# Kernel optimization log

Hardware: AMD Instinct MI355X
Metric: run time of the kernel (lower is better)

The kernel has to match this reference:

```python
import jax, jax.numpy as jnp
import numpy as np

BLOCK = 64          # block_size
R = 64              # number of OFT blocks (r)
N_ELEM = BLOCK * (BLOCK - 1) // 2  # 2016 upper-triangular elements per block
TOKENS = 8192       # batch*seq tokens
IN_FEATURES = R * BLOCK  # 4096
NUM_TERMS = 5       # num_cayley_neumann_terms

_ROWS, _COLS = jnp.triu_indices(BLOCK, k=1)


def _skew_symmetric(vec):
    # vec: [r, n_elements] -> [r, BLOCK, BLOCK] skew-symmetric
    m = jnp.zeros((vec.shape[0], BLOCK, BLOCK), dtype=vec.dtype)
    m = m.at[:, _ROWS, _COLS].set(vec)
    return m - jnp.swapaxes(m, -2, -1)


def _cayley_neumann(weight):
    # Neumann approximation of Cayley transform:
    # R = I + 2*Q + 2*Q^2 + ... + 2*Q^(NUM_TERMS-1)
    Q = _skew_symmetric(weight)                      # [r, B, B]
    eye = jnp.eye(BLOCK, dtype=weight.dtype)
    rot = eye[None, :, :] + 2.0 * Q
    Q_pow = Q
    for _ in range(2, NUM_TERMS):
        Q_pow = jnp.einsum('rij,rjk->rik', Q_pow, Q)
        rot = rot + 2.0 * Q_pow
    return rot                                        # [r, B, B]


def setup_inputs() -> dict:
    key = jax.random.key(0)
    k1, k2 = jax.random.split(key)
    x = jax.random.normal(k1, (TOKENS, IN_FEATURES), dtype=jnp.float32)
    # OFT weights start near zero (rotation ~ identity); small scale keeps
    # the Neumann series well-conditioned.
    weight = jax.random.normal(k2, (R, N_ELEM), dtype=jnp.float32) * 0.02
    return {"x": x, "weight": weight}


def reference(x, weight):
    rot = _cayley_neumann(weight)                      # [r, B, B]
    xr = x.reshape(x.shape[0], R, BLOCK)               # [n, r, B]
    out = jnp.einsum('nrk,rkc->nrc', xr, rot)          # block-diag rotation
    return out.reshape(x.shape)
```

## Files before the change

### kernel.cpp

```cpp
#include <hip/hip_runtime.h>


#define NELEM 2016

typedef __attribute__((ext_vector_type(8))) short bfrag8;
typedef __attribute__((ext_vector_type(4))) float f32x4;

__device__ __forceinline__ int triu_off(int i) {
    return i * 63 - (i * (i - 1)) / 2;
}

__device__ __forceinline__ float skew_val(const float* __restrict__ wr, int i, int j) {
    if (i < j) return  wr[triu_off(i) + (j - i - 1)];
    if (i > j) return -wr[triu_off(j) + (i - j - 1)];
    return 0.f;
}

__device__ __forceinline__ void bsplit(float v, short& h, short& l) {
    const unsigned u = __float_as_uint(v);
    h = (short)(u >> 16);
    const float resid = v - __uint_as_float(u & 0xffff0000u);
    const unsigned ur = __float_as_uint(resid);
    l = (short)((ur + 0x7fffu + ((ur >> 16) & 1u)) >> 16);
}

__global__ __launch_bounds__(256) void oft_rot_kernel(const float* __restrict__ w,
                                                      unsigned short* __restrict__ bh,
                                                      unsigned short* __restrict__ bl) {
    __shared__ float Q[64][64];
    __shared__ float Pl[2][16][65];

    const int r    = blockIdx.x;
    const int tile = blockIdx.y;
    const float* __restrict__ wr = w + r * NELEM;
    const int tid = threadIdx.x;
    const int il  = tid >> 4;
    const int j0  = (tid & 15) << 2;
    const int gi  = tile * 16 + il;

#pragma unroll
    for (int m = 0; m < 4; ++m) {
        const int i = il + 16 * m;
#pragma unroll
        for (int t = 0; t < 4; ++t)
            Q[i][j0 + t] = skew_val(wr, i, j0 + t);
    }
    __syncthreads();

    float racc[4];
#pragma unroll
    for (int t = 0; t < 4; ++t) {
        const float qv = Q[gi][j0 + t];
        Pl[0][il][j0 + t] = qv;
        racc[t] = (gi == j0 + t ? 1.f : 0.f) + 2.f * qv;
    }
    __syncthreads();

    int cur = 0;
#pragma unroll
    for (int p = 2; p < 5; ++p) {
        float a0 = 0.f, a1 = 0.f, a2 = 0.f, a3 = 0.f;
#pragma unroll 8
        for (int k = 0; k < 64; ++k) {
            const float  pv = Pl[cur][il][k];
            const float4 qv = *(const float4*)&Q[k][j0];
            a0 = fmaf(pv, qv.x, a0);
            a1 = fmaf(pv, qv.y, a1);
            a2 = fmaf(pv, qv.z, a2);
            a3 = fmaf(pv, qv.w, a3);
        }
        Pl[cur ^ 1][il][j0 + 0] = a0;
        Pl[cur ^ 1][il][j0 + 1] = a1;
        Pl[cur ^ 1][il][j0 + 2] = a2;
        Pl[cur ^ 1][il][j0 + 3] = a3;
        racc[0] += 2.f * a0;
        racc[1] += 2.f * a1;
        racc[2] += 2.f * a2;
        racc[3] += 2.f * a3;
        __syncthreads();
        cur ^= 1;
    }

    const int s    = gi >> 5;
    const int jj   = gi & 7;
    const int lhi  = ((gi >> 3) & 3) << 4;
#pragma unroll
    for (int t = 0; t < 4; ++t) {
        const int j    = j0 + t;
        const int ct   = j >> 4;
        const int lane = lhi + (j & 15);
        const int off  = (((r * 4 + ct) * 2 + s) * 64 + lane) * 8 + jj;
        short h, l;
        bsplit(racc[t], h, l);
        bh[off] = (unsigned short)h;
        bl[off] = (unsigned short)l;
    }
}

__global__ __launch_bounds__(256) void oft_apply_kernel(const float* __restrict__ x,
                                                        const unsigned short* __restrict__ bh,
                                                        const unsigned short* __restrict__ bl,
                                                        float* __restrict__ out) {
    const int tid  = threadIdx.x;
    const int w    = tid >> 6;
    const int l    = tid & 63;
    const int lrow = l & 15;
    const int lk   = l >> 4;
    const int r     = blockIdx.x;
    const int chunk = blockIdx.y;

    bfrag8 Bh[4][2], Bl[4][2];
#pragma unroll
    for (int ct = 0; ct < 4; ++ct)
#pragma unroll
        for (int s = 0; s < 2; ++s) {
            const int off = (((r * 4 + ct) * 2 + s) * 64 + l) * 8;
            Bh[ct][s] = *(const bfrag8*)(bh + off);
            Bl[ct][s] = *(const bfrag8*)(bl + off);
        }

#pragma unroll
    for (int tt = 0; tt < 4; ++tt) {
        const int tokbase = (chunk * 4 + tt) * 64 + w * 16;
        const float* __restrict__ xp =
            x + (size_t)(tokbase + lrow) * 4096 + r * 64 + lk * 8;

        const f32x4 a0 = *(const f32x4*)(xp);
        const f32x4 a1 = *(const f32x4*)(xp + 4);
        const f32x4 a2 = *(const f32x4*)(xp + 32);
        const f32x4 a3 = *(const f32x4*)(xp + 36);

        bfrag8 Ah0, Al0, Ah1, Al1;
#pragma unroll
        for (int j = 0; j < 4; ++j) {
            short h, lo;
            bsplit(a0[j], h, lo); Ah0[j]     = h; Al0[j]     = lo;
            bsplit(a1[j], h, lo); Ah0[4 + j] = h; Al0[4 + j] = lo;
            bsplit(a2[j], h, lo); Ah1[j]     = h; Al1[j]     = lo;
            bsplit(a3[j], h, lo); Ah1[4 + j] = h; Al1[4 + j] = lo;
        }

        f32x4 acc[4];
#pragma unroll
        for (int ct = 0; ct < 4; ++ct) {
            acc[ct] = (f32x4)(0.f);
            acc[ct] = __builtin_amdgcn_mfma_f32_16x16x32_bf16(Al0, Bh[ct][0], acc[ct], 0, 0, 0);
            acc[ct] = __builtin_amdgcn_mfma_f32_16x16x32_bf16(Ah0, Bl[ct][0], acc[ct], 0, 0, 0);
            acc[ct] = __builtin_amdgcn_mfma_f32_16x16x32_bf16(Ah0, Bh[ct][0], acc[ct], 0, 0, 0);
            acc[ct] = __builtin_amdgcn_mfma_f32_16x16x32_bf16(Al1, Bh[ct][1], acc[ct], 0, 0, 0);
            acc[ct] = __builtin_amdgcn_mfma_f32_16x16x32_bf16(Ah1, Bl[ct][1], acc[ct], 0, 0, 0);
            acc[ct] = __builtin_amdgcn_mfma_f32_16x16x32_bf16(Ah1, Bh[ct][1], acc[ct], 0, 0, 0);
        }

        const size_t obase = (size_t)(tokbase + lk * 4) * 4096 + r * 64 + lrow;
#pragma unroll
        for (int ct = 0; ct < 4; ++ct)
#pragma unroll
            for (int q = 0; q < 4; ++q)
                out[obase + (size_t)q * 4096 + ct * 16] = acc[ct][q];
    }
}

extern "C" void kernel_launch(void* const* d_in, const int* in_sizes, int n_in,
                              void* d_out, int out_size, void* d_ws, size_t ws_size,
                              hipStream_t stream) {
    const float* x = (const float*)d_in[0];
    const float* w = (const float*)d_in[1];
    float* out = (float*)d_out;

    unsigned short* bh = (unsigned short*)d_ws;
    unsigned short* bl = bh + 64 * 4 * 2 * 64 * 8;

    oft_rot_kernel<<<dim3(64, 4), 256, 0, stream>>>(w, bh, bl);
    oft_apply_kernel<<<dim3(64, 32), 256, 0, stream>>>(x, bh, bl, out);
}
```

Baseline: 253.6 us.

## Stage outputs through LDS for vectorized stores and prefetch next x tile

The apply kernel now writes MFMA accumulators to a per-wave shared-memory tile and reads them back as float4 rows, so global stores become 16-byte coalesced writes instead of scattered scalar stores. It also software-prefetches the next token tile's x fragment before issuing MFMAs, and doubles the work per block (8 tiles, half the grid) with a launch-bounds occupancy hint. Risks are added LDS traffic, reliance on a manual lgkmcnt wait instead of a barrier for intra-wave visibility, and reduced grid parallelism.

```diff
diff --git a/kernel.cpp b/kernel.cpp
--- a/kernel.cpp
+++ b/kernel.cpp
@@ -81,9 +81,9 @@
         cur ^= 1;
     }
 
-    const int s    = gi >> 5;
-    const int jj   = gi & 7;
-    const int lhi  = ((gi >> 3) & 3) << 4;
+    const int s   = gi >> 5;
+    const int jj  = gi & 7;
+    const int lhi = ((gi >> 3) & 3) << 4;
 #pragma unroll
     for (int t = 0; t < 4; ++t) {
         const int j    = j0 + t;
@@ -97,10 +97,12 @@
     }
 }
 
-__global__ __launch_bounds__(256) void oft_apply_kernel(const float* __restrict__ x,
-                                                        const unsigned short* __restrict__ bh,
-                                                        const unsigned short* __restrict__ bl,
-                                                        float* __restrict__ out) {
+__global__ __launch_bounds__(256, 4) void oft_apply_kernel(const float* __restrict__ x,
+                                                           const unsigned short* __restrict__ bh,
+                                                           const unsigned short* __restrict__ bl,
+                                                           float* __restrict__ out) {
+    __shared__ float ots[4][2][16][68];
+
     const int tid  = threadIdx.x;
     const int w    = tid >> 6;
     const int l    = tid & 63;
@@ -119,17 +121,16 @@
             Bl[ct][s] = *(const bfrag8*)(bl + off);
         }
 
+    const int tok0 = chunk * 512 + w * 16;
+    const float* __restrict__ xp = x + (size_t)(tok0 + lrow) * 4096 + (size_t)r * 64 + lk * 8;
+
+    f32x4 a0 = *(const f32x4*)(xp);
+    f32x4 a1 = *(const f32x4*)(xp + 4);
+    f32x4 a2 = *(const f32x4*)(xp + 32);
+    f32x4 a3 = *(const f32x4*)(xp + 36);
+
 #pragma unroll
-    for (int tt = 0; tt < 4; ++tt) {
-        const int tokbase = (chunk * 4 + tt) * 64 + w * 16;
-        const float* __restrict__ xp =
-            x + (size_t)(tokbase + lrow) * 4096 + r * 64 + lk * 8;
-
-        const f32x4 a0 = *(const f32x4*)(xp);
-        const f32x4 a1 = *(const f32x4*)(xp + 4);
-        const f32x4 a2 = *(const f32x4*)(xp + 32);
-        const f32x4 a3 = *(const f32x4*)(xp + 36);
-
+    for (int t = 0; t < 8; ++t) {
         bfrag8 Ah0, Al0, Ah1, Al1;
 #pragma unroll
         for (int j = 0; j < 4; ++j) {
@@ -138,6 +139,14 @@
             bsplit(a1[j], h, lo); Ah0[4 + j] = h; Al0[4 + j] = lo;
             bsplit(a2[j], h, lo); Ah1[j]     = h; Al1[j]     = lo;
             bsplit(a3[j], h, lo); Ah1[4 + j] = h; Al1[4 + j] = lo;
+        }
+
+        if (t < 7) {
+            const float* __restrict__ xq = xp + (size_t)(t + 1) * 64 * 4096;
+            a0 = *(const f32x4*)(xq);
+            a1 = *(const f32x4*)(xq + 4);
+            a2 = *(const f32x4*)(xq + 32);
+            a3 = *(const f32x4*)(xq + 36);
         }
 
         f32x4 acc[4];
@@ -152,12 +161,25 @@
             acc[ct] = __builtin_amdgcn_mfma_f32_16x16x32_bf16(Ah1, Bh[ct][1], acc[ct], 0, 0, 0);
         }
 
-        const size_t obase = (size_t)(tokbase + lk * 4) * 4096 + r * 64 + lrow;
+        float* otw = &ots[w][t & 1][0][0];
 #pragma unroll
         for (int ct = 0; ct < 4; ++ct)
 #pragma unroll
             for (int q = 0; q < 4; ++q)
-                out[obase + (size_t)q * 4096 + ct * 16] = acc[ct][q];
+                otw[(lk * 4 + q) * 68 + ct * 16 + lrow] = acc[ct][q];
+
+        asm volatile("s_waitcnt lgkmcnt(0)" ::: "memory");
+
+        const int tokt = tok0 + t * 64;
+#pragma unroll
+        for (int v = 0; v < 2; ++v)
+#pragma unroll
+            for (int half = 0; half < 2; ++half) {
+                const int row = v * 8 + (l >> 3);
+                const int cf  = half * 32 + (l & 7) * 4;
+                const f32x4 d = *(const f32x4*)&otw[row * 68 + cf];
+                *(f32x4*)(out + (size_t)(tokt + row) * 4096 + (size_t)r * 64 + cf) = d;
+            }
     }
 }
 
@@ -172,5 +194,5 @@
     unsigned short* bl = bh + 64 * 4 * 2 * 64 * 8;
 
     oft_rot_kernel<<<dim3(64, 4), 256, 0, stream>>>(w, bh, bl);
-    oft_apply_kernel<<<dim3(64, 32), 256, 0, stream>>>(x, bh, bl, out);
+    oft_apply_kernel<<<dim3(64, 16), 256, 0, stream>>>(x, bh, bl, out);
 }
```

New measurement: 254.8 us. About the same (+0.5%).
